# Kernel optimization log

Measured on AMD Instinct MI355X. Metric: run time of the kernel, lower is better.

## Reference

```python
import jax, jax.numpy as jnp
import numpy as np

B, L, D, H = 4, 512, 256, 128  # batch, seq_len, input_size, hidden_size
NEG = -1e30


def setup_inputs() -> dict:
    key = jax.random.key(0)
    ks = jax.random.split(key, 16)
    init = lambda k, shape, fan_in: (jax.random.normal(k, shape, jnp.float32) / np.sqrt(fan_in).astype(np.float32))
    v = jax.random.normal(ks[0], (B, L, D), jnp.float32)
    lengths = jax.random.randint(ks[1], (B,), L // 2, L + 1).astype(jnp.int32)
    p_mask = (jnp.arange(L)[None, :] < lengths[:, None])  # [B, L] bool
    return {
        "v": v,
        "lengths": lengths,
        "p_mask": p_mask,
        "own_W": init(ks[2], (H, D), D), "own_b": jnp.zeros((H,), jnp.float32),
        "comp_W": init(ks[3], (H, D), D), "comp_b": jnp.zeros((H,), jnp.float32),
        "v_attn": init(ks[4], (H,), H),
        "gate_W": init(ks[5], (2 * D, 2 * D), 2 * D), "gate_b": jnp.zeros((2 * D,), jnp.float32),
        "w_ih_f": init(ks[6], (3 * H, 2 * D), 2 * D), "w_hh_f": init(ks[7], (3 * H, H), H),
        "b_ih_f": jnp.zeros((3 * H,), jnp.float32), "b_hh_f": jnp.zeros((3 * H,), jnp.float32),
        "w_ih_b": init(ks[8], (3 * H, 2 * D), 2 * D), "w_hh_b": init(ks[9], (3 * H, H), H),
        "b_ih_b": jnp.zeros((3 * H,), jnp.float32), "b_hh_b": jnp.zeros((3 * H,), jnp.float32),
    }


def _gru(x, tmask, w_ih, w_hh, b_ih, b_hh, reverse):
    """Single-direction GRU over [B, L, In] with length masking (emulates packing)."""
    Bn, Ln, _ = x.shape
    Hn = w_hh.shape[1]
    xp = jnp.einsum('bli,hi->blh', x, w_ih) + b_ih  # [B, L, 3H] input projections

    def step(h, inputs):
        xpt, m = inputs  # [B, 3H], [B, 1]
        hp = h @ w_hh.T + b_hh
        xr, xz, xn = jnp.split(xpt, 3, axis=-1)
        hr, hz, hn = jnp.split(hp, 3, axis=-1)
        r = jax.nn.sigmoid(xr + hr)
        z = jax.nn.sigmoid(xz + hz)
        n = jnp.tanh(xn + r * hn)
        h_new = (1.0 - z) * n + z * h
        h = jnp.where(m, h_new, h)
        return h, jnp.where(m, h_new, jnp.zeros_like(h_new))

    h0 = jnp.zeros((Bn, Hn), x.dtype)
    xs = (jnp.swapaxes(xp, 0, 1), tmask.T[:, :, None])
    _, outs = jax.lax.scan(step, h0, xs, reverse=reverse)
    return jnp.swapaxes(outs, 0, 1)  # [B, L, H]


def reference(v, lengths, p_mask, own_W, own_b, comp_W, comp_b, v_attn,
              gate_W, gate_b, w_ih_f, w_hh_f, b_ih_f, b_hh_f,
              w_ih_b, w_hh_b, b_ih_b, b_hh_b):
    # Additive (Bahdanau / RNet) self-attention, vectorized over all query positions.
    own = v @ own_W.T + own_b    # [B, L, H] (query term)
    comp = v @ comp_W.T + comp_b  # [B, L, H] (key term)
    # scores[b, q, k] = tanh(own_q + comp_k) . v_attn
    scores = jnp.einsum('bqkh,h->bqk', jnp.tanh(own[:, :, None, :] + comp[:, None, :, :]), v_attn)
    scores = jnp.where(p_mask[:, None, :], scores, NEG)  # mask padded keys
    attn = jax.nn.softmax(scores, axis=2)
    C = jnp.einsum('bqk,bkd->bqd', attn, v)  # attended context
    inp = jnp.concatenate([v, C], axis=-1)   # [B, L, 2D]
    inp = jax.nn.sigmoid(inp @ gate_W.T + gate_b) * inp  # gating
    # Bidirectional GRU encoder (pack_padded emulated via time mask; eval mode, no dropout).
    tmask = (jnp.arange(inp.shape[1])[None, :] < lengths[:, None])
    out_f = _gru(inp, tmask, w_ih_f, w_hh_f, b_ih_f, b_hh_f, reverse=False)
    out_b = _gru(inp, tmask, w_ih_b, w_hh_b, b_ih_b, b_hh_b, reverse=True)
    return jnp.concatenate([out_f, out_b], axis=-1)  # [B, L, 2H]
```

## Files before the change

kernel.cpp:

```cpp
#include <hip/hip_runtime.h>
#include <hip/hip_bf16.h>

#define NEGINF -1e30f

typedef __attribute__((ext_vector_type(8))) short short8;
typedef __attribute__((ext_vector_type(4))) float f32x4;
typedef __attribute__((ext_vector_type(4))) int int4_t;

__device__ __forceinline__ float fast_sigmoid(float x) {
    return __builtin_amdgcn_rcpf(1.f + __expf(-x));
}
__device__ __forceinline__ float fast_tanh(float x) {
    return 1.f - 2.f * __builtin_amdgcn_rcpf(1.f + __expf(2.f * x));
}
__device__ __forceinline__ short f2bf(float f) {
    unsigned u = __float_as_uint(f);
    return (short)((u + 0x7fff + ((u >> 16) & 1)) >> 16);
}
__device__ __forceinline__ float bf2f(short b) {
    return __uint_as_float(((unsigned)(unsigned short)b) << 16);
}

__device__ __forceinline__ void bar_lds() {
    asm volatile("s_waitcnt lgkmcnt(0)\n\ts_barrier" ::: "memory");
}

__global__ __launch_bounds__(256) void gemm_bias(
    const float* __restrict__ A,
    const float* __restrict__ W1, const float* __restrict__ b1, float* __restrict__ out1,
    const float* __restrict__ W2, const float* __restrict__ b2, float* __restrict__ out2,
    const int* __restrict__ lengths,
    int M, int N, int K, int nsplit, int mode) {
    const int m0 = blockIdx.y * 64;
    if ((m0 & 511) >= lengths[m0 >> 9]) return;
    __shared__ __align__(16) short Abh[2][2048];
    __shared__ __align__(16) short Abl[2][2048];
    __shared__ __align__(16) short Bbh[2][2048];
    __shared__ __align__(16) short Bbl[2][2048];
    const int tid = threadIdx.x;
    int bx = blockIdx.x;
    const float* W = W1; const float* bias = b1; float* out = out1;
    int n0;
    if (bx < nsplit) {
        n0 = bx * 64;
    } else {
        W = W2; bias = b2; out = out2;
        n0 = (bx - nsplit) * 64;
    }
    const int wave = tid >> 6;
    const int lane = tid & 63;
    const int mrow = lane & 15;
    const int quad = lane >> 4;
    const int wm = (wave >> 1) * 32;
    const int wn = (wave & 1) * 32;

    const int r_ = tid >> 2;
    const int sg = (tid & 3) * 8;

    f32x4 acc[2][2];
#pragma unroll
    for (int mt = 0; mt < 2; mt++)
#pragma unroll
        for (int nt = 0; nt < 2; nt++) acc[mt][nt] = (f32x4){0.f, 0.f, 0.f, 0.f};

    float4 a0 = *(const float4*)(A + (size_t)(m0 + r_) * K + sg);
    float4 a1 = *(const float4*)(A + (size_t)(m0 + r_) * K + sg + 4);
    float4 w0 = *(const float4*)(W + (size_t)(n0 + r_) * K + sg);
    float4 w1 = *(const float4*)(W + (size_t)(n0 + r_) * K + sg + 4);

    for (int k0 = 0; k0 < K; k0 += 32) {
        const int cur = (k0 >> 5) & 1;
        {
            float av[8] = {a0.x, a0.y, a0.z, a0.w, a1.x, a1.y, a1.z, a1.w};
            float wv[8] = {w0.x, w0.y, w0.z, w0.w, w1.x, w1.y, w1.z, w1.w};
            short8 ah, al, bh, bl;
#pragma unroll
            for (int j = 0; j < 8; j++) {
                short h = f2bf(av[j]); ah[j] = h; al[j] = f2bf(av[j] - bf2f(h));
                short g = f2bf(wv[j]); bh[j] = g; bl[j] = f2bf(wv[j] - bf2f(g));
            }
            *(short8*)&Abh[cur][r_ * 32 + sg] = ah;
            *(short8*)&Abl[cur][r_ * 32 + sg] = al;
            *(short8*)&Bbh[cur][r_ * 32 + sg] = bh;
            *(short8*)&Bbl[cur][r_ * 32 + sg] = bl;
        }
        if (k0 + 32 < K) {
            a0 = *(const float4*)(A + (size_t)(m0 + r_) * K + k0 + 32 + sg);
            a1 = *(const float4*)(A + (size_t)(m0 + r_) * K + k0 + 32 + sg + 4);
            w0 = *(const float4*)(W + (size_t)(n0 + r_) * K + k0 + 32 + sg);
            w1 = *(const float4*)(W + (size_t)(n0 + r_) * K + k0 + 32 + sg + 4);
        }
        bar_lds();
        short8 Ah[2], Al[2], Bh[2], Bl[2];
#pragma unroll
        for (int t = 0; t < 2; t++) {
            int ar = (wm + t * 16 + mrow) * 32 + quad * 8;
            int br = (wn + t * 16 + mrow) * 32 + quad * 8;
            Ah[t] = *(const short8*)&Abh[cur][ar];
            Al[t] = *(const short8*)&Abl[cur][ar];
            Bh[t] = *(const short8*)&Bbh[cur][br];
            Bl[t] = *(const short8*)&Bbl[cur][br];
        }
#pragma unroll
        for (int mt = 0; mt < 2; mt++)
#pragma unroll
            for (int nt = 0; nt < 2; nt++) {
                acc[mt][nt] = __builtin_amdgcn_mfma_f32_16x16x32_bf16(Ah[mt], Bh[nt], acc[mt][nt], 0, 0, 0);
                acc[mt][nt] = __builtin_amdgcn_mfma_f32_16x16x32_bf16(Al[mt], Bh[nt], acc[mt][nt], 0, 0, 0);
                acc[mt][nt] = __builtin_amdgcn_mfma_f32_16x16x32_bf16(Ah[mt], Bl[nt], acc[mt][nt], 0, 0, 0);
            }
        bar_lds();
    }
    float bsv[2];
#pragma unroll
    for (int nt = 0; nt < 2; nt++) bsv[nt] = bias[n0 + wn + nt * 16 + mrow];
#pragma unroll
    for (int mt = 0; mt < 2; mt++)
#pragma unroll
        for (int nt = 0; nt < 2; nt++) {
            int n = n0 + wn + nt * 16 + mrow;
#pragma unroll
            for (int r = 0; r < 4; r++) {
                int m = m0 + wm + mt * 16 + quad * 4 + r;
                float val = acc[mt][nt][r] + bsv[nt];
                if (mode == 1) val = fast_sigmoid(val) * A[(size_t)m * K + n];
                out[(size_t)m * N + n] = val;
            }
        }
}

__global__ __launch_bounds__(512) void attn_kernel(
    const float* __restrict__ v, const int* __restrict__ lengths,
    const float* __restrict__ own, const float* __restrict__ comp,
    const float* __restrict__ v_attn, float* __restrict__ inp) {
    const int L = 512, D = 256, H = 128;
    const int b = blockIdx.x >> 6;
    const int q0 = (blockIdx.x & 63) * 8;
    const int len = lengths[b];
    if (q0 >= len) return;
    const int tid = threadIdx.x;
    const float K2E = 2.8853900817779268f;
    __shared__ __align__(16) float oKT[128 * 8];
    __shared__ float va2s[128];
    __shared__ __align__(16) float scf[512 * 12];
    __shared__ float inv8[8];

    for (int i = tid; i < 1024; i += 512) {
        int qq = i >> 7, hh = i & 127;
        oKT[hh * 8 + qq] = K2E * own[((size_t)(b * L + q0 + qq)) * H + hh];
    }
    if (tid < 128) va2s[tid] = -2.f * v_attn[tid];
    __syncthreads();

    {
        const int k = tid;
        float acc[8];
#pragma unroll
        for (int q = 0; q < 8; q++) acc[q] = 0.f;
        if (k < len) {
            const float* cp = comp + ((size_t)(b * L + k)) * H;
            for (int h = 0; h < 128; h += 4) {
                float4 c4 = *(const float4*)(cp + h);
                const float* cv = (const float*)&c4;
#pragma unroll
                for (int j = 0; j < 4; j++) {
                    float cK = cv[j] * K2E;
                    float va = va2s[h + j];
                    float4 o0 = *(const float4*)&oKT[(h + j) * 8];
                    float4 o1 = *(const float4*)&oKT[(h + j) * 8 + 4];
                    const float* op0 = (const float*)&o0;
                    const float* op1 = (const float*)&o1;
#pragma unroll
                    for (int q = 0; q < 4; q++) {
                        float r = __builtin_amdgcn_rcpf(1.f + exp2f(cK + op0[q]));
                        acc[q] = fmaf(va, r, acc[q]);
                    }
#pragma unroll
                    for (int q = 0; q < 4; q++) {
                        float r = __builtin_amdgcn_rcpf(1.f + exp2f(cK + op1[q]));
                        acc[4 + q] = fmaf(va, r, acc[4 + q]);
                    }
                }
            }
#pragma unroll
            for (int q = 0; q < 8; q++) acc[q] = __expf(acc[q]);
        }
        *(float4*)&scf[k * 12] = *(float4*)&acc[0];
        *(float4*)&scf[k * 12 + 4] = *(float4*)&acc[4];
    }
    __syncthreads();

    {
        int w = tid >> 6, l = tid & 63;
        float s = 0.f;
#pragma unroll
        for (int kk = 0; kk < 8; kk++) s += scf[(l + kk * 64) * 12 + w];
#pragma unroll
        for (int off = 1; off < 64; off <<= 1) s += __shfl_xor(s, off);
        if (l == 0) inv8[w] = __builtin_amdgcn_rcpf(s);
    }
    __syncthreads();

    {
        const int d = tid & 255;
        const int qh = tid >> 8;
        float c0 = 0.f, c1 = 0.f, c2 = 0.f, c3 = 0.f;
        const float* vb = v + ((size_t)b * L) * D + d;
        for (int k = 0; k < L; k += 2) {
            float v0 = vb[(size_t)k * D];
            float v1 = vb[(size_t)(k + 1) * D];
            float4 s0 = *(const float4*)&scf[k * 12 + qh * 4];
            float4 s1 = *(const float4*)&scf[(k + 1) * 12 + qh * 4];
            c0 += s0.x * v0 + s1.x * v1;
            c1 += s0.y * v0 + s1.y * v1;
            c2 += s0.z * v0 + s1.z * v1;
            c3 += s0.w * v0 + s1.w * v1;
        }
        float cc[4] = {c0, c1, c2, c3};
#pragma unroll
        for (int j = 0; j < 4; j++) {
            int q = q0 + qh * 4 + j;
            size_t row = ((size_t)(b * L + q)) * 512;
            inp[row + 256 + d] = cc[j] * inv8[qh * 4 + j];
            inp[row + d] = v[((size_t)(b * L + q)) * D + d];
        }
    }
}

__global__ __launch_bounds__(512, 1) void gru_kernel(
    const float* __restrict__ xp_f, const float* __restrict__ xp_b,
    const float* __restrict__ w_hh_f, const float* __restrict__ w_hh_b,
    const float* __restrict__ b_hh_f, const float* __restrict__ b_hh_b,
    const int* __restrict__ lengths, float* __restrict__ out) {
    const int L = 512, H = 128;
    const int dir = blockIdx.x >> 2;
    const int b = blockIdx.x & 3;
    const float* xp = dir ? xp_b : xp_f;
    const float* w_hh = dir ? w_hh_b : w_hh_f;
    const float* b_hh = dir ? b_hh_b : b_hh_f;
    const int tid = threadIdx.x;
    const int wave = tid >> 6;
    const int lane = tid & 63;
    const int mrow = lane & 15;
    const int quad = lane >> 4;
    const int jj = 16 * wave + lane;

    __shared__ __align__(16) signed char hbufc[2][384];

    int4_t wb[3][2];
    float ws[3];
#pragma unroll
    for (int g = 0; g < 3; g++) {
        int row = g * 128 + 16 * wave + mrow;
        float wv[32];
#pragma unroll
        for (int kt = 0; kt < 2; kt++)
#pragma unroll
            for (int j4 = 0; j4 < 4; j4++) {
                float4 f4 = *(const float4*)(w_hh + (size_t)row * H + kt * 64 + quad * 16 + j4 * 4);
                wv[kt * 16 + j4 * 4 + 0] = f4.x;
                wv[kt * 16 + j4 * 4 + 1] = f4.y;
                wv[kt * 16 + j4 * 4 + 2] = f4.z;
                wv[kt * 16 + j4 * 4 + 3] = f4.w;
            }
        float mx = 0.f;
#pragma unroll
        for (int j = 0; j < 32; j++) mx = fmaxf(mx, fabsf(wv[j]));
        mx = fmaxf(mx, __shfl_xor(mx, 16));
        mx = fmaxf(mx, __shfl_xor(mx, 32));
        mx = fmaxf(mx, 1e-30f);
        float inv_s = 127.f / mx;
        ws[g] = (mx / 127.f) * (1.f / 8192.f);
#pragma unroll
        for (int kt = 0; kt < 2; kt++) {
            int tmp[4] = {0, 0, 0, 0};
#pragma unroll
            for (int j = 0; j < 16; j++) {
                int q = (int)rintf(wv[kt * 16 + j] * inv_s);
                tmp[j >> 2] |= (q & 0xff) << ((j & 3) * 8);
            }
            wb[g][kt] = (int4_t){tmp[0], tmp[1], tmp[2], tmp[3]};
        }
    }
    float br = 0.f, bz = 0.f, bn = 0.f, hcur = 0.f;
    if (lane < 16) {
        br = b_hh[jj];
        bz = b_hh[128 + jj];
        bn = b_hh[256 + jj];
    }

    const int len = lengths[b];
    for (int i = tid; i < (L - len) * 128; i += 512) {
        int tt = len + (i >> 7);
        int kk = i & 127;
        out[((size_t)(b * L + tt)) * 256 + dir * 128 + kk] = 0.f;
    }
    for (int i = tid; i < 768; i += 512) ((signed char*)hbufc)[i] = 0;

    const int nch = (len + 15) >> 4;
    float xr[16], xz[16], xn[16];
    if (lane < 16) {
#pragma unroll
        for (int s = 0; s < 16; s++) {
            if (s < len) {
                int t = dir ? (len - 1 - s) : s;
                size_t base = ((size_t)(b * L + t)) * 384;
                xr[s] = xp[base + jj];
                xz[s] = xp[base + 128 + jj];
                xn[s] = xp[base + 256 + jj];
            }
        }
    }
    __syncthreads();

    const int bbase = ((mrow & 1) ? 192 : 0) + quad * 16;
    int par = 0;

    for (int c = 0; c < nch; c++) {
        const int cnt = min(16, len - c * 16);
        float nxr[16], nxz[16], nxn[16];
        if (lane < 16 && c + 1 < nch) {
#pragma unroll
            for (int s = 0; s < 16; s++) {
                int rr = (c + 1) * 16 + s;
                if (rr < len) {
                    int t = dir ? (len - 1 - rr) : rr;
                    size_t base = ((size_t)(b * L + t)) * 384;
                    nxr[s] = xp[base + jj];
                    nxz[s] = xp[base + 128 + jj];
                    nxn[s] = xp[base + 256 + jj];
                }
            }
        }
#pragma unroll
        for (int s = 0; s < 16; s++) {
            if (s < cnt) {
                int4_t af0 = *(const int4_t*)&hbufc[par][bbase];
                int4_t af1 = *(const int4_t*)&hbufc[par][bbase + 64];
                int4_t a0 = (int4_t){0, 0, 0, 0};
                int4_t a1 = (int4_t){0, 0, 0, 0};
                int4_t a2 = (int4_t){0, 0, 0, 0};
                a0 = __builtin_amdgcn_mfma_i32_16x16x64_i8(af0, wb[0][0], a0, 0, 0, 0);
                a0 = __builtin_amdgcn_mfma_i32_16x16x64_i8(af1, wb[0][1], a0, 0, 0, 0);
                a1 = __builtin_amdgcn_mfma_i32_16x16x64_i8(af0, wb[1][0], a1, 0, 0, 0);
                a1 = __builtin_amdgcn_mfma_i32_16x16x64_i8(af1, wb[1][1], a1, 0, 0, 0);
                a2 = __builtin_amdgcn_mfma_i32_16x16x64_i8(af0, wb[2][0], a2, 0, 0, 0);
                a2 = __builtin_amdgcn_mfma_i32_16x16x64_i8(af1, wb[2][1], a2, 0, 0, 0);
                if (lane < 16) {
                    float r = fast_sigmoid(fmaf((float)(a0[0] * 64 + a0[1]), ws[0], xr[s] + br));
                    float z = fast_sigmoid(fmaf((float)(a1[0] * 64 + a1[1]), ws[1], xz[s] + bz));
                    float hh = fmaf((float)(a2[0] * 64 + a2[1]), ws[2], bn);
                    float n = fast_tanh(xn[s] + r * hh);
                    float hn = (1.f - z) * n + z * hcur;
                    hcur = hn;
                    float hs = fminf(fmaxf(hn * 8192.f, -8191.f), 8191.f);
                    int h13 = (int)rintf(hs);
                    int hi = h13 >> 6;
                    int lo = h13 - (hi << 6);
                    hbufc[par ^ 1][jj] = (signed char)hi;
                    hbufc[par ^ 1][192 + jj] = (signed char)lo;
                    int t = dir ? (len - 1 - (c * 16 + s)) : (c * 16 + s);
                    out[((size_t)(b * L + t)) * 256 + dir * 128 + jj] = hn;
                }
                par ^= 1;
                bar_lds();
            }
        }
        if (lane < 16 && c + 1 < nch) {
#pragma unroll
            for (int s = 0; s < 16; s++) { xr[s] = nxr[s]; xz[s] = nxz[s]; xn[s] = nxn[s]; }
        }
    }
}

extern "C" void kernel_launch(void* const* d_in, const int* in_sizes, int n_in,
                              void* d_out, int out_size, void* d_ws, size_t ws_size,
                              hipStream_t stream) {
    const int B = 4, L = 512, D = 256, H = 128;
    const int M = B * L;

    const float* v      = (const float*)d_in[0];
    const int* lengths  = (const int*)d_in[1];
    const float* own_W  = (const float*)d_in[3];
    const float* own_b  = (const float*)d_in[4];
    const float* comp_W = (const float*)d_in[5];
    const float* comp_b = (const float*)d_in[6];
    const float* v_attn = (const float*)d_in[7];
    const float* gate_W = (const float*)d_in[8];
    const float* gate_b = (const float*)d_in[9];
    const float* w_ih_f = (const float*)d_in[10];
    const float* w_hh_f = (const float*)d_in[11];
    const float* b_ih_f = (const float*)d_in[12];
    const float* b_hh_f = (const float*)d_in[13];
    const float* w_ih_b = (const float*)d_in[14];
    const float* w_hh_b = (const float*)d_in[15];
    const float* b_ih_b = (const float*)d_in[16];
    const float* b_hh_b = (const float*)d_in[17];

    float* ws   = (float*)d_ws;
    float* own  = ws;
    float* comp = own + (size_t)M * H;
    float* inp  = comp + (size_t)M * H;
    float* gated = inp + (size_t)M * 512;
    float* xp_f = gated + (size_t)M * 512;
    float* xp_b = xp_f + (size_t)M * 384;
    float* out  = (float*)d_out;

    gemm_bias<<<dim3(4, M / 64), 256, 0, stream>>>(
        v, own_W, own_b, own, comp_W, comp_b, comp, lengths, M, H, D, 2, 0);
    attn_kernel<<<dim3(B * 64), 512, 0, stream>>>(v, lengths, own, comp, v_attn, inp);
    gemm_bias<<<dim3(8, M / 64), 256, 0, stream>>>(
        inp, gate_W, gate_b, gated, gate_W, gate_b, gated, lengths, M, 512, 512, 8, 1);
    gemm_bias<<<dim3(12, M / 64), 256, 0, stream>>>(
        gated, w_ih_f, b_ih_f, xp_f, w_ih_b, b_ih_b, xp_b, lengths, M, 384, 512, 6, 0);
    gru_kernel<<<dim3(8), 512, 0, stream>>>(xp_f, xp_b, w_hh_f, w_hh_b, b_hh_f, b_hh_b, lengths, out);
}
```

Measured before the change: 354.1 us.

## Fuse forward and backward GRU directions into one block per batch

Each GRU block now runs both the forward and backward recurrences for one batch element, so the grid drops from 8 to 4 blocks. The two independent chains share one barrier per step, and their MFMA and activation work can interleave to hide latency on the serial path. The prefetch chunk is halved from 16 to 8 steps to limit register pressure from the doubled state. Per-step work per block roughly doubles, which could lengthen each step if the two directions' instructions do not overlap well.

```diff
diff --git a/kernel.cpp b/kernel.cpp
--- a/kernel.cpp
+++ b/kernel.cpp
@@ -233,11 +233,7 @@
     const float* __restrict__ b_hh_f, const float* __restrict__ b_hh_b,
     const int* __restrict__ lengths, float* __restrict__ out) {
     const int L = 512, H = 128;
-    const int dir = blockIdx.x >> 2;
-    const int b = blockIdx.x & 3;
-    const float* xp = dir ? xp_b : xp_f;
-    const float* w_hh = dir ? w_hh_b : w_hh_f;
-    const float* b_hh = dir ? b_hh_b : b_hh_f;
+    const int b = blockIdx.x;
     const int tid = threadIdx.x;
     const int wave = tid >> 6;
     const int lane = tid & 63;
@@ -245,69 +241,77 @@
     const int quad = lane >> 4;
     const int jj = 16 * wave + lane;
 
-    __shared__ __align__(16) signed char hbufc[2][384];
-
-    int4_t wb[3][2];
-    float ws[3];
-#pragma unroll
-    for (int g = 0; g < 3; g++) {
-        int row = g * 128 + 16 * wave + mrow;
-        float wv[32];
-#pragma unroll
-        for (int kt = 0; kt < 2; kt++)
-#pragma unroll
-            for (int j4 = 0; j4 < 4; j4++) {
-                float4 f4 = *(const float4*)(w_hh + (size_t)row * H + kt * 64 + quad * 16 + j4 * 4);
-                wv[kt * 16 + j4 * 4 + 0] = f4.x;
-                wv[kt * 16 + j4 * 4 + 1] = f4.y;
-                wv[kt * 16 + j4 * 4 + 2] = f4.z;
-                wv[kt * 16 + j4 * 4 + 3] = f4.w;
-            }
-        float mx = 0.f;
-#pragma unroll
-        for (int j = 0; j < 32; j++) mx = fmaxf(mx, fabsf(wv[j]));
-        mx = fmaxf(mx, __shfl_xor(mx, 16));
-        mx = fmaxf(mx, __shfl_xor(mx, 32));
-        mx = fmaxf(mx, 1e-30f);
-        float inv_s = 127.f / mx;
-        ws[g] = (mx / 127.f) * (1.f / 8192.f);
-#pragma unroll
-        for (int kt = 0; kt < 2; kt++) {
-            int tmp[4] = {0, 0, 0, 0};
-#pragma unroll
-            for (int j = 0; j < 16; j++) {
-                int q = (int)rintf(wv[kt * 16 + j] * inv_s);
-                tmp[j >> 2] |= (q & 0xff) << ((j & 3) * 8);
-            }
-            wb[g][kt] = (int4_t){tmp[0], tmp[1], tmp[2], tmp[3]};
-        }
-    }
-    float br = 0.f, bz = 0.f, bn = 0.f, hcur = 0.f;
+    __shared__ __align__(16) signed char hbufc[2][2][384];
+
+    int4_t wb[2][3][2];
+    float ws[2][3];
+#pragma unroll
+    for (int d = 0; d < 2; d++) {
+        const float* w_hh = d ? w_hh_b : w_hh_f;
+#pragma unroll
+        for (int g = 0; g < 3; g++) {
+            int row = g * 128 + 16 * wave + mrow;
+            float wv[32];
+#pragma unroll
+            for (int kt = 0; kt < 2; kt++)
+#pragma unroll
+                for (int j4 = 0; j4 < 4; j4++) {
+                    float4 f4 = *(const float4*)(w_hh + (size_t)row * H + kt * 64 + quad * 16 + j4 * 4);
+                    wv[kt * 16 + j4 * 4 + 0] = f4.x;
+                    wv[kt * 16 + j4 * 4 + 1] = f4.y;
+                    wv[kt * 16 + j4 * 4 + 2] = f4.z;
+                    wv[kt * 16 + j4 * 4 + 3] = f4.w;
+                }
+            float mx = 0.f;
+#pragma unroll
+            for (int j = 0; j < 32; j++) mx = fmaxf(mx, fabsf(wv[j]));
+            mx = fmaxf(mx, __shfl_xor(mx, 16));
+            mx = fmaxf(mx, __shfl_xor(mx, 32));
+            mx = fmaxf(mx, 1e-30f);
+            float inv_s = 127.f / mx;
+            ws[d][g] = (mx / 127.f) * (1.f / 8192.f);
+#pragma unroll
+            for (int kt = 0; kt < 2; kt++) {
+                int tmp[4] = {0, 0, 0, 0};
+#pragma unroll
+                for (int j = 0; j < 16; j++) {
+                    int q = (int)rintf(wv[kt * 16 + j] * inv_s);
+                    tmp[j >> 2] |= (q & 0xff) << ((j & 3) * 8);
+                }
+                wb[d][g][kt] = (int4_t){tmp[0], tmp[1], tmp[2], tmp[3]};
+            }
+        }
+    }
+    float br[2], bz[2], bn[2], hcur[2];
+    hcur[0] = hcur[1] = 0.f;
     if (lane < 16) {
-        br = b_hh[jj];
-        bz = b_hh[128 + jj];
-        bn = b_hh[256 + jj];
+#pragma unroll
+        for (int d = 0; d < 2; d++) {
+            const float* b_hh = d ? b_hh_b : b_hh_f;
+            br[d] = b_hh[jj];
+            bz[d] = b_hh[128 + jj];
+            bn[d] = b_hh[256 + jj];
+        }
     }
 
     const int len = lengths[b];
-    for (int i = tid; i < (L - len) * 128; i += 512) {
-        int tt = len + (i >> 7);
-        int kk = i & 127;
-        out[((size_t)(b * L + tt)) * 256 + dir * 128 + kk] = 0.f;
-    }
-    for (int i = tid; i < 768; i += 512) ((signed char*)hbufc)[i] = 0;
-
-    const int nch = (len + 15) >> 4;
-    float xr[16], xz[16], xn[16];
+    for (int i = tid; i < (L - len) * 256; i += 512) {
+        int tt = len + (i >> 8);
+        int kk = i & 255;
+        out[((size_t)(b * L + tt)) * 256 + kk] = 0.f;
+    }
+    for (int i = tid; i < 1536; i += 512) ((signed char*)hbufc)[i] = 0;
+
+    const int nch = (len + 7) >> 3;
+    float xf0[8], xf1[8], xf2[8], xb0[8], xb1[8], xb2[8];
     if (lane < 16) {
 #pragma unroll
-        for (int s = 0; s < 16; s++) {
+        for (int s = 0; s < 8; s++) {
             if (s < len) {
-                int t = dir ? (len - 1 - s) : s;
-                size_t base = ((size_t)(b * L + t)) * 384;
-                xr[s] = xp[base + jj];
-                xz[s] = xp[base + 128 + jj];
-                xn[s] = xp[base + 256 + jj];
+                size_t bf = ((size_t)(b * L + s)) * 384;
+                size_t bb = ((size_t)(b * L + (len - 1 - s))) * 384;
+                xf0[s] = xp_f[bf + jj]; xf1[s] = xp_f[bf + 128 + jj]; xf2[s] = xp_f[bf + 256 + jj];
+                xb0[s] = xp_b[bb + jj]; xb1[s] = xp_b[bb + 128 + jj]; xb2[s] = xp_b[bb + 256 + jj];
             }
         }
     }
@@ -317,50 +321,65 @@
     int par = 0;
 
     for (int c = 0; c < nch; c++) {
-        const int cnt = min(16, len - c * 16);
-        float nxr[16], nxz[16], nxn[16];
+        const int cnt = min(8, len - c * 8);
+        float nf0[8], nf1[8], nf2[8], nb0[8], nb1[8], nb2[8];
         if (lane < 16 && c + 1 < nch) {
 #pragma unroll
-            for (int s = 0; s < 16; s++) {
-                int rr = (c + 1) * 16 + s;
+            for (int s = 0; s < 8; s++) {
+                int rr = (c + 1) * 8 + s;
                 if (rr < len) {
-                    int t = dir ? (len - 1 - rr) : rr;
-                    size_t base = ((size_t)(b * L + t)) * 384;
-                    nxr[s] = xp[base + jj];
-                    nxz[s] = xp[base + 128 + jj];
-                    nxn[s] = xp[base + 256 + jj];
-                }
-            }
-        }
-#pragma unroll
-        for (int s = 0; s < 16; s++) {
+                    size_t bf = ((size_t)(b * L + rr)) * 384;
+                    size_t bb = ((size_t)(b * L + (len - 1 - rr))) * 384;
+                    nf0[s] = xp_f[bf + jj]; nf1[s] = xp_f[bf + 128 + jj]; nf2[s] = xp_f[bf + 256 + jj];
+                    nb0[s] = xp_b[bb + jj]; nb1[s] = xp_b[bb + 128 + jj]; nb2[s] = xp_b[bb + 256 + jj];
+                }
+            }
+        }
+#pragma unroll
+        for (int s = 0; s < 8; s++) {
             if (s < cnt) {
-                int4_t af0 = *(const int4_t*)&hbufc[par][bbase];
-                int4_t af1 = *(const int4_t*)&hbufc[par][bbase + 64];
-                int4_t a0 = (int4_t){0, 0, 0, 0};
-                int4_t a1 = (int4_t){0, 0, 0, 0};
-                int4_t a2 = (int4_t){0, 0, 0, 0};
-                a0 = __builtin_amdgcn_mfma_i32_16x16x64_i8(af0, wb[0][0], a0, 0, 0, 0);
-                a0 = __builtin_amdgcn_mfma_i32_16x16x64_i8(af1, wb[0][1], a0, 0, 0, 0);
-                a1 = __builtin_amdgcn_mfma_i32_16x16x64_i8(af0, wb[1][0], a1, 0, 0, 0);
-                a1 = __builtin_amdgcn_mfma_i32_16x16x64_i8(af1, wb[1][1], a1, 0, 0, 0);
-                a2 = __builtin_amdgcn_mfma_i32_16x16x64_i8(af0, wb[2][0], a2, 0, 0, 0);
-                a2 = __builtin_amdgcn_mfma_i32_16x16x64_i8(af1, wb[2][1], a2, 0, 0, 0);
+                int4_t aff0 = *(const int4_t*)&hbufc[0][par][bbase];
+                int4_t aff1 = *(const int4_t*)&hbufc[0][par][bbase + 64];
+                int4_t afb0 = *(const int4_t*)&hbufc[1][par][bbase];
+                int4_t afb1 = *(const int4_t*)&hbufc[1][par][bbase + 64];
+                int4_t a[2][3];
+#pragma unroll
+                for (int d = 0; d < 2; d++)
+#pragma unroll
+                    for (int g = 0; g < 3; g++) a[d][g] = (int4_t){0, 0, 0, 0};
+#pragma unroll
+                for (int g = 0; g < 3; g++) {
+                    a[0][g] = __builtin_amdgcn_mfma_i32_16x16x64_i8(aff0, wb[0][g][0], a[0][g], 0, 0, 0);
+                    a[0][g] = __builtin_amdgcn_mfma_i32_16x16x64_i8(aff1, wb[0][g][1], a[0][g], 0, 0, 0);
+                    a[1][g] = __builtin_amdgcn_mfma_i32_16x16x64_i8(afb0, wb[1][g][0], a[1][g], 0, 0, 0);
+                    a[1][g] = __builtin_amdgcn_mfma_i32_16x16x64_i8(afb1, wb[1][g][1], a[1][g], 0, 0, 0);
+                }
                 if (lane < 16) {
-                    float r = fast_sigmoid(fmaf((float)(a0[0] * 64 + a0[1]), ws[0], xr[s] + br));
-                    float z = fast_sigmoid(fmaf((float)(a1[0] * 64 + a1[1]), ws[1], xz[s] + bz));
-                    float hh = fmaf((float)(a2[0] * 64 + a2[1]), ws[2], bn);
-                    float n = fast_tanh(xn[s] + r * hh);
-                    float hn = (1.f - z) * n + z * hcur;
-                    hcur = hn;
-                    float hs = fminf(fmaxf(hn * 8192.f, -8191.f), 8191.f);
-                    int h13 = (int)rintf(hs);
-                    int hi = h13 >> 6;
-                    int lo = h13 - (hi << 6);
-                    hbufc[par ^ 1][jj] = (signed char)hi;
-                    hbufc[par ^ 1][192 + jj] = (signed char)lo;
-                    int t = dir ? (len - 1 - (c * 16 + s)) : (c * 16 + s);
-                    out[((size_t)(b * L + t)) * 256 + dir * 128 + jj] = hn;
+                    float rf = fast_sigmoid(fmaf((float)(a[0][0][0] * 64 + a[0][0][1]), ws[0][0], xf0[s] + br[0]));
+                    float zf = fast_sigmoid(fmaf((float)(a[0][1][0] * 64 + a[0][1][1]), ws[0][1], xf1[s] + bz[0]));
+                    float hhf = fmaf((float)(a[0][2][0] * 64 + a[0][2][1]), ws[0][2], bn[0]);
+                    float rb = fast_sigmoid(fmaf((float)(a[1][0][0] * 64 + a[1][0][1]), ws[1][0], xb0[s] + br[1]));
+                    float zb = fast_sigmoid(fmaf((float)(a[1][1][0] * 64 + a[1][1][1]), ws[1][1], xb1[s] + bz[1]));
+                    float hhb = fmaf((float)(a[1][2][0] * 64 + a[1][2][1]), ws[1][2], bn[1]);
+                    float nf = fast_tanh(xf2[s] + rf * hhf);
+                    float nb = fast_tanh(xb2[s] + rb * hhb);
+                    float hnf = (1.f - zf) * nf + zf * hcur[0];
+                    float hnb = (1.f - zb) * nb + zb * hcur[1];
+                    hcur[0] = hnf;
+                    hcur[1] = hnb;
+                    float hsf = fminf(fmaxf(hnf * 8192.f, -8191.f), 8191.f);
+                    float hsb = fminf(fmaxf(hnb * 8192.f, -8191.f), 8191.f);
+                    int h13f = (int)rintf(hsf);
+                    int h13b = (int)rintf(hsb);
+                    int hif = h13f >> 6, lof = h13f - (hif << 6);
+                    int hib = h13b >> 6, lob = h13b - (hib << 6);
+                    hbufc[0][par ^ 1][jj] = (signed char)hif;
+                    hbufc[0][par ^ 1][192 + jj] = (signed char)lof;
+                    hbufc[1][par ^ 1][jj] = (signed char)hib;
+                    hbufc[1][par ^ 1][192 + jj] = (signed char)lob;
+                    int t = c * 8 + s;
+                    out[((size_t)(b * L + t)) * 256 + jj] = hnf;
+                    out[((size_t)(b * L + (len - 1 - t))) * 256 + 128 + jj] = hnb;
                 }
                 par ^= 1;
                 bar_lds();
@@ -368,7 +387,10 @@
         }
         if (lane < 16 && c + 1 < nch) {
 #pragma unroll
-            for (int s = 0; s < 16; s++) { xr[s] = nxr[s]; xz[s] = nxz[s]; xn[s] = nxn[s]; }
+            for (int s = 0; s < 8; s++) {
+                xf0[s] = nf0[s]; xf1[s] = nf1[s]; xf2[s] = nf2[s];
+                xb0[s] = nb0[s]; xb1[s] = nb1[s]; xb2[s] = nb2[s];
+            }
         }
     }
 }
@@ -413,5 +435,5 @@
         inp, gate_W, gate_b, gated, gate_W, gate_b, gated, lengths, M, 512, 512, 8, 1);
     gemm_bias<<<dim3(12, M / 64), 256, 0, stream>>>(
         gated, w_ih_f, b_ih_f, xp_f, w_ih_b, b_ih_b, xp_b, lengths, M, 384, 512, 6, 0);
-    gru_kernel<<<dim3(8), 512, 0, stream>>>(xp_f, xp_b, w_hh_f, w_hh_b, b_hh_f, b_hh_b, lengths, out);
-}
+    gru_kernel<<<dim3(4), 512, 0, stream>>>(xp_f, xp_b, w_hh_f, w_hh_b, b_hh_f, b_hh_b, lengths, out);
+}
```

Result: slower. 457.8 us (+29.3%).
